# Optimization experiments

Hardware: AMD Instinct MI355X
Metric: run time of the kernel (lower is better)

Reference implementation:

```python
import jax, jax.numpy as jnp
import numpy as np
from jax import lax

DN = ('NCHW', 'OIHW', 'NCHW')

def conv(x, w, b, stride=1, pad=0):
    y = lax.conv_general_dilated(x, w, (stride, stride), ((pad, pad), (pad, pad)), dimension_numbers=DN)
    return y + b[None, :, None, None]

def conv_transpose(x, w, b):
    # torch ConvTranspose2d(k=4, s=2, p=1): w is (in_ch, out_ch, 4, 4)
    wf = jnp.flip(w, (2, 3)).transpose(1, 0, 2, 3)  # -> (out_ch, in_ch, 4, 4)
    pad = 4 - 1 - 1  # k - 1 - p = 2
    y = lax.conv_general_dilated(x, wf, (1, 1), ((pad, pad), (pad, pad)), lhs_dilation=(2, 2), dimension_numbers=DN)
    return y + b[None, :, None, None]

def setup_inputs() -> dict:
    key = jax.random.key(0)
    ks = jax.random.split(key, 16)
    HID, ZC, K = 256, 64, 512
    def w(k, shape):
        return (jax.random.normal(k, shape, jnp.float32) * 0.02)
    z = lambda n: jnp.zeros((n,), jnp.float32)
    return {
        'x': jax.random.uniform(ks[0], (8, 3, 128, 128), jnp.float32),
        'c1_w': w(ks[1], (HID, 3, 4, 4)), 'c1_b': z(HID),
        'c2_w': w(ks[2], (HID, HID, 4, 4)), 'c2_b': z(HID),
        'r0_w3': w(ks[3], (HID, HID, 3, 3)), 'r0_b3': z(HID),
        'r0_w1': w(ks[4], (HID, HID, 1, 1)), 'r0_b1': z(HID),
        'r1_w3': w(ks[5], (HID, HID, 3, 3)), 'r1_b3': z(HID),
        'r1_w1': w(ks[6], (HID, HID, 1, 1)), 'r1_b1': z(HID),
        'to_z_w': w(ks[7], (ZC, HID, 1, 1)), 'to_z_b': z(ZC),
        'codebook': jax.random.uniform(ks[8], (K, ZC), jnp.float32, -1.0 / K, 1.0 / K),
        'from_z_w': w(ks[9], (HID, ZC, 1, 1)), 'from_z_b': z(HID),
        't1_w': w(ks[10], (HID, HID, 4, 4)), 't1_b': z(HID),
        't2_w': w(ks[11], (HID, 3, 4, 4)), 't2_b': z(3),
    }

def _vqvae(x, c1_w, c1_b, c2_w, c2_b, r0_w3, r0_b3, r0_w1, r0_b1,
           r1_w3, r1_b3, r1_w1, r1_b1, to_z_w, to_z_b, codebook,
           from_z_w, from_z_b, t1_w, t1_b, t2_w, t2_b):
    # ---- Encoder ----
    h = jax.nn.relu(conv(x, c1_w, c1_b, stride=2, pad=1))
    h = jax.nn.relu(conv(h, c2_w, c2_b, stride=2, pad=1))
    for (w3, b3, w1, b1) in ((r0_w3, r0_b3, r0_w1, r0_b1), (r1_w3, r1_b3, r1_w1, r1_b1)):
        r = conv(jax.nn.relu(h), w3, b3, pad=1)
        r = conv(jax.nn.relu(r), w1, b1)
        h = h + r
    z_e = conv(h, to_z_w, to_z_b)  # [B, ZC, H/4, W/4]
    # ---- Vector quantization ----
    B, C, H, W = z_e.shape
    z_flat = z_e.transpose(0, 2, 3, 1).reshape(-1, C)  # [N, C]
    dist = (jnp.sum(z_flat * z_flat, axis=1, keepdims=True)
            - 2.0 * z_flat @ codebook.T
            + jnp.sum(codebook * codebook, axis=1)[None, :])  # [N, K]
    ids = jnp.argmin(dist, axis=1)  # [N]
    e_k_flat = codebook[ids]  # [N, C]
    e_k_st_flat = z_flat + lax.stop_gradient(e_k_flat - z_flat)
    e_k = e_k_flat.reshape(B, H, W, C).transpose(0, 3, 1, 2)
    e_k_st = e_k_st_flat.reshape(B, H, W, C).transpose(0, 3, 1, 2)
    ids = ids.reshape(B, H, W)
    # ---- Decoder ----
    d = jax.nn.relu(conv(e_k_st, from_z_w, from_z_b))
    d = jax.nn.relu(conv_transpose(d, t1_w, t1_b))
    out = jax.nn.sigmoid(conv_transpose(d, t2_w, t2_b))
    return out, z_e, e_k, ids

def reference(x, c1_w, c1_b, c2_w, c2_b, r0_w3, r0_b3, r0_w1, r0_b1,
              r1_w3, r1_b3, r1_w1, r1_b1, to_z_w, to_z_b, codebook,
              from_z_w, from_z_b, t1_w, t1_b, t2_w, t2_b):
    return _vqvae(x, c1_w, c1_b, c2_w, c2_b, r0_w3, r0_b3, r0_w1, r0_b1,
                  r1_w3, r1_b3, r1_w1, r1_b1, to_z_w, to_z_b, codebook,
                  from_z_w, from_z_b, t1_w, t1_b, t2_w, t2_b)
```

## Files before the change

kernel.cpp:

```cpp
#include <hip/hip_runtime.h>
#include <math.h>


typedef unsigned int uint;
typedef unsigned short ushort_t;
using short8 = __attribute__((ext_vector_type(8))) short;
using f32x4  = __attribute__((ext_vector_type(4))) float;

__device__ __attribute__((aligned(16))) ushort_t g_zpad[512];

static __device__ __forceinline__ int rfl(int x) { return __builtin_amdgcn_readfirstlane(x); }
static __device__ __forceinline__ ushort_t f2bf(float f) {
  uint u = __float_as_uint(f);
  return (ushort_t)((u + 0x7fffu + ((u >> 16) & 1u)) >> 16);
}
static __device__ __forceinline__ float bf2f(ushort_t b) {
  return __uint_as_float(((uint)b) << 16);
}
static __device__ __forceinline__ void gload16(const ushort_t* g, void* l) {
  __builtin_amdgcn_global_load_lds(
      (const __attribute__((address_space(1))) void*)g,
      (__attribute__((address_space(3))) void*)l, 16, 0, 0);
}

__global__ __launch_bounds__(256) void k_prep_misc(
    const float* __restrict__ c1w, float* __restrict__ wt_c1,
    const float* __restrict__ tozw, float* __restrict__ wt_toz,
    const float* __restrict__ fromzw, float* __restrict__ wt_fromz,
    const float* __restrict__ cb, float* __restrict__ cnorm,
    const float* __restrict__ t2w, ushort_t* __restrict__ w2pk)
{
  const int b = blockIdx.x, tid = threadIdx.x;
  if (b < 48) {
    int idx = b * 256 + tid;
    int co = idx % 256, i = idx / 256;
    wt_c1[idx] = c1w[co * 48 + i];
  } else if (b < 112) {
    int idx = (b - 48) * 256 + tid;
    int co = idx % 64, i = idx / 64;
    wt_toz[idx] = tozw[co * 256 + i];
  } else if (b < 176) {
    int idx = (b - 112) * 256 + tid;
    int co = idx % 256, i = idx / 256;
    wt_fromz[idx] = fromzw[co * 64 + i];
  } else if (b < 178) {
    int idx = (b - 176) * 256 + tid;
    if (idx < 512) {
      float s = 0.f;
      for (int c = 0; c < 64; ++c) { float v = cb[idx * 64 + c]; s = fmaf(v, v, s); }
      cnorm[idx] = s;
    }
  } else {
    int idx = (b - 178) * 256 + tid;
    int k = idx & 31, co = (idx >> 5) & 15, chunk = (idx >> 9) & 31, par = idx >> 14;
    int tap = chunk >> 3, cg = chunk & 7;
    int a = tap >> 1, bb = tap & 1;
    int ry = par & 1, rx = (par >> 1) & 1;
    int ky = ((ry + 1) & 1) + 2 * a;
    int kx = ((rx + 1) & 1) + 2 * bb;
    int ci = cg * 32 + k;
    float v = (co < 3) ? t2w[((ci * 3 + co) << 4) + ky * 4 + kx] : 0.f;
    w2pk[idx] = f2bf(v);
  }
}

template<int KIND>
__global__ __launch_bounds__(256) void k_prep_enc(
    const float* __restrict__ w, ushort_t* __restrict__ wp)
{
  constexpr int KK = (KIND == 0) ? 16 : (KIND == 1 ? 9 : 1);
  constexpr int KW = (KIND == 0) ? 4  : (KIND == 1 ? 3 : 1);
  constexpr int NT = KK;
  const int tid = threadIdx.x;
  const int wvg = blockIdx.x * 4 + (tid >> 6);
  const int lane = tid & 63;
  const int co = wvg >> 2;
  const int ci = (wvg & 3) * 64 + lane;
  const float* src = w + (size_t)(co * 256 + ci) * KK;
  const int coT = co >> 6, row = co & 63, cg = ci >> 5, k = ci & 31;
  float v[KK];
#pragma unroll
  for (int j = 0; j < KK; ++j) v[j] = src[j];
#pragma unroll
  for (int tap = 0; tap < NT; ++tap) {
    int ky, kx;
    if (KIND == 0)      { ky = tap >> 2; kx = tap & 3; }
    else if (KIND == 1) { ky = tap / 3;  kx = tap - ky * 3; }
    else                { ky = 0; kx = 0; }
    float val = v[ky * KW + kx];
    ushort_t b0 = f2bf(val);
    ushort_t b1 = f2bf(val - bf2f(b0));
    const int chunk = tap * 8 + cg;
    size_t base = ((size_t)(chunk * 4 + coT) << 12) + row * 32 + k;
    wp[base] = b0;
    wp[base + 2048] = b1;
  }
}

template<int KIND>
__global__ __launch_bounds__(256) void k_prep_enc2(
    const float* __restrict__ wa, ushort_t* __restrict__ oa,
    const float* __restrict__ wb2, ushort_t* __restrict__ ob)
{
  constexpr int KK = (KIND == 0) ? 16 : (KIND == 1 ? 9 : 1);
  constexpr int KW = (KIND == 0) ? 4  : (KIND == 1 ? 3 : 1);
  constexpr int NT = KK;
  const float* w = (blockIdx.x < 256) ? wa : wb2;
  ushort_t* wp = (blockIdx.x < 256) ? oa : ob;
  const int bx = blockIdx.x & 255;
  const int tid = threadIdx.x;
  const int wvg = bx * 4 + (tid >> 6);
  const int lane = tid & 63;
  const int co = wvg >> 2;
  const int ci = (wvg & 3) * 64 + lane;
  const float* src = w + (size_t)(co * 256 + ci) * KK;
  const int coT = co >> 6, row = co & 63, cg = ci >> 5, k = ci & 31;
  float v[KK];
#pragma unroll
  for (int j = 0; j < KK; ++j) v[j] = src[j];
#pragma unroll
  for (int tap = 0; tap < NT; ++tap) {
    int ky, kx;
    if (KIND == 0)      { ky = tap >> 2; kx = tap & 3; }
    else if (KIND == 1) { ky = tap / 3;  kx = tap - ky * 3; }
    else                { ky = 0; kx = 0; }
    float val = v[ky * KW + kx];
    ushort_t b0 = f2bf(val);
    ushort_t b1 = f2bf(val - bf2f(b0));
    const int chunk = tap * 8 + cg;
    size_t base = ((size_t)(chunk * 4 + coT) << 12) + row * 32 + k;
    wp[base] = b0;
    wp[base + 2048] = b1;
  }
}

__global__ void k_prep_t1w(const float* __restrict__ w, ushort_t* __restrict__ wb) {
  int idx = blockIdx.x * 256 + threadIdx.x;
  int kk  = idx & 31;
  int co  = (idx >> 5) & 255;
  int c8  = (idx >> 13) & 7;
  int tap = (idx >> 16) & 3;
  int par = idx >> 18;
  int ry = par & 1, rx = (par >> 1) & 1;
  int a = tap >> 1, b = tap & 1;
  int ky = ((ry + 1) & 1) + 2 * a;
  int kx = ((rx + 1) & 1) + 2 * b;
  int ci = c8 * 32 + kk;
  wb[idx] = f2bf(w[((ci * 256 + co) << 4) + ky * 4 + kx]);
}

__global__ __launch_bounds__(256) void k_conv1_split(
    const float* __restrict__ in, ushort_t* __restrict__ o0, ushort_t* __restrict__ o1,
    const float* __restrict__ wT, const float* __restrict__ bias)
{
  __shared__ float s_in[3 * 360];
  const int tid = threadIdx.x;
  const int lane = tid & 63;
  const int wv = rfl(tid >> 6);
  const int px = lane & 7, py = lane >> 3;
  const int tx = blockIdx.x & 7, ty = blockIdx.x >> 3;
  const int X = tx * 8, Y = ty * 8;
  const int cob = blockIdx.y * 64 + wv * 16;
  const int n = blockIdx.z;
  float acc[16];
#pragma unroll
  for (int i = 0; i < 16; ++i) acc[i] = bias[cob + i];
  const float* inN = in + (size_t)n * 3 * 16384;
  for (int e = tid; e < 3 * 360; e += 256) {
    int col2 = e % 20; int t = e / 20; int row = t % 18; int ci = t / 18;
    int pr = col2 / 10, hc = col2 % 10, ixl = 2 * hc + pr;
    int iy = 2 * Y - 1 + row, ix = 2 * X - 1 + ixl;
    float v = 0.f;
    if (ixl < 18 && (unsigned)iy < 128u && (unsigned)ix < 128u)
      v = inN[ci * 16384 + iy * 128 + ix];
    s_in[e] = v;
  }
  __syncthreads();
  const float* wc = wT + cob;
#pragma unroll
  for (int c = 0; c < 3; ++c) {
    const float* base = s_in + c * 360 + py * 40 + px;
#pragma unroll
    for (int ky = 0; ky < 4; ++ky) {
#pragma unroll
      for (int kx = 0; kx < 4; ++kx) {
        float iv = base[ky * 20 + (kx & 1) * 10 + (kx >> 1)];
        const float* w = wc + (size_t)(c * 16 + ky * 4 + kx) * 256;
#pragma unroll
        for (int i = 0; i < 16; ++i) acc[i] = fmaf(iv, w[i], acc[i]);
      }
    }
  }
  const int pxg = n * 4096 + (Y + py) * 64 + (X + px);
  uint p0[8], p1[8];
#pragma unroll
  for (int i = 0; i < 8; ++i) {
    float va = fmaxf(acc[2 * i], 0.f), vb = fmaxf(acc[2 * i + 1], 0.f);
    ushort_t a0 = f2bf(va), b0 = f2bf(vb);
    ushort_t a1 = f2bf(va - bf2f(a0)), b1 = f2bf(vb - bf2f(b0));
    p0[i] = (uint)a0 | ((uint)b0 << 16);
    p1[i] = (uint)a1 | ((uint)b1 << 16);
  }
  ushort_t* d0 = o0 + (size_t)pxg * 256 + cob;
  ushort_t* d1 = o1 + (size_t)pxg * 256 + cob;
  uint4 v0a; v0a.x = p0[0]; v0a.y = p0[1]; v0a.z = p0[2]; v0a.w = p0[3];
  uint4 v0b; v0b.x = p0[4]; v0b.y = p0[5]; v0b.z = p0[6]; v0b.w = p0[7];
  uint4 v1a; v1a.x = p1[0]; v1a.y = p1[1]; v1a.z = p1[2]; v1a.w = p1[3];
  uint4 v1b; v1b.x = p1[4]; v1b.y = p1[5]; v1b.z = p1[6]; v1b.w = p1[7];
  *(uint4*)d0 = v0a; *(uint4*)(d0 + 8) = v0b;
  *(uint4*)d1 = v1a; *(uint4*)(d1 + 8) = v1b;
}

template<int KIND>
__global__ __launch_bounds__(256) void k_enc_mfma_split(
    const ushort_t* __restrict__ x0, const ushort_t* __restrict__ x1,
    const ushort_t* __restrict__ wp, float* __restrict__ part)
{
  __shared__ ushort_t smem[2][12288];
  const int tid = threadIdx.x, lane = tid & 63, wv = tid >> 6;
  const int l15 = lane & 15, q = lane >> 4;
  const int pxT = blockIdx.x, coT = blockIdx.y;
  constexpr int NCH = (KIND == 0) ? 128 : 72;
  const int CH0 = blockIdx.z * (NCH / 2), CH1 = CH0 + NCH / 2;
  f32x4 acc[4][2];
#pragma unroll
  for (int m = 0; m < 4; ++m)
#pragma unroll
    for (int n = 0; n < 2; ++n) acc[m][n] = (f32x4){0.f, 0.f, 0.f, 0.f};

  const int r0 = tid >> 2, kq = tid & 3;
  int bimg[2], bu[2], bvc[2];
#pragma unroll
  for (int r = 0; r < 2; ++r) {
    int bpx = pxT * 128 + r0 + r * 64;
    bimg[r] = bpx >> 10; int bp = bpx & 1023; bu[r] = bp >> 5; bvc[r] = bp & 31;
  }
  const ushort_t* srcB[2][2];
  int ptap = -1;
  auto retap = [&](int tap) {
    ptap = tap;
    int ky, kx;
    if (KIND == 0) { ky = tap >> 2; kx = tap & 3; }
    else           { ky = tap / 3;  kx = tap - ky * 3; }
#pragma unroll
    for (int r = 0; r < 2; ++r) {
      bool v; size_t rowb;
      if (KIND == 0) {
        int iy = 2 * bu[r] - 1 + ky, ix = 2 * bvc[r] - 1 + kx;
        v = ((unsigned)iy < 64u) && ((unsigned)ix < 64u);
        rowb = ((size_t)(bimg[r] * 4096 + iy * 64 + ix)) << 8;
      } else {
        int iy = bu[r] - 1 + ky, ix = bvc[r] - 1 + kx;
        v = ((unsigned)iy < 32u) && ((unsigned)ix < 32u);
        rowb = ((size_t)(bimg[r] * 1024 + iy * 32 + ix)) << 8;
      }
      srcB[r][0] = (v ? (x0 + rowb) : g_zpad) + kq * 8;
      srcB[r][1] = (v ? (x1 + rowb) : g_zpad) + kq * 8;
    }
  };

  const int wvb = wv * 1024;
  auto stage = [&](int chunk, int bi) {
    const int tap = chunk >> 3, cg = chunk & 7;
    if (tap != ptap) retap(tap);
    char* bufb = (char*)smem[bi];
    const ushort_t* ap = wp + ((size_t)(chunk * 4 + coT) << 12) + tid * 8;
    gload16(ap,        bufb + wvb);
    gload16(ap + 2048, bufb + 4096 + wvb);
    const int ko = cg * 32;
    gload16(srcB[0][0] + ko, bufb + 8192 + wvb);
    gload16(srcB[1][0] + ko, bufb + 8192 + 4096 + wvb);
    gload16(srcB[0][1] + ko, bufb + 16384 + wvb);
    gload16(srcB[1][1] + ko, bufb + 16384 + 4096 + wvb);
  };
  auto compute = [&](const ushort_t* buf) {
    const ushort_t* sA = buf;
    const ushort_t* sB = buf + 4096;
    short8 af[4][2], bf[2][2];
#pragma unroll
    for (int m = 0; m < 4; ++m)
#pragma unroll
      for (int pl = 0; pl < 2; ++pl)
        af[m][pl] = *(const short8*)(sA + pl * 2048 + (m * 16 + l15) * 32 + q * 8);
#pragma unroll
    for (int n = 0; n < 2; ++n)
#pragma unroll
      for (int pl = 0; pl < 2; ++pl)
        bf[n][pl] = *(const short8*)(sB + pl * 4096 + (wv * 32 + n * 16 + l15) * 32 + q * 8);
#pragma unroll
    for (int m = 0; m < 4; ++m)
#pragma unroll
      for (int n = 0; n < 2; ++n) {
        acc[m][n] = __builtin_amdgcn_mfma_f32_16x16x32_bf16(af[m][0], bf[n][0], acc[m][n], 0, 0, 0);
        acc[m][n] = __builtin_amdgcn_mfma_f32_16x16x32_bf16(af[m][0], bf[n][1], acc[m][n], 0, 0, 0);
        acc[m][n] = __builtin_amdgcn_mfma_f32_16x16x32_bf16(af[m][1], bf[n][0], acc[m][n], 0, 0, 0);
      }
  };

  stage(CH0, 0);
  __syncthreads();
  int cur = 0;
  for (int c = CH0; c < CH1; ++c) {
    if (c + 1 < CH1) stage(c + 1, cur ^ 1);
    compute(smem[cur]);
    __syncthreads();
    cur ^= 1;
  }

  float* pz = part + ((size_t)blockIdx.z << 21);
#pragma unroll
  for (int m = 0; m < 4; ++m) {
#pragma unroll
    for (int n = 0; n < 2; ++n) {
#pragma unroll
      for (int r = 0; r < 4; ++r) {
        const int co_l = m * 16 + q * 4 + r;
        const int px_l = wv * 32 + n * 16 + l15;
        const int px = pxT * 128 + px_l;
        const int img = px >> 10, pp = px & 1023;
        const size_t ha = ((size_t)(img * 256 + coT * 64 + co_l)) * 1024 + pp;
        pz[ha] = acc[m][n][r];
      }
    }
  }
}

__global__ __launch_bounds__(256) void k_enc_mfma_3x3f(
    const ushort_t* __restrict__ x0, const ushort_t* __restrict__ x1,
    const ushort_t* __restrict__ wp, const float* __restrict__ bias,
    ushort_t* __restrict__ s0, ushort_t* __restrict__ s1)
{
  __shared__ ushort_t smem[32768];
  const int tid = threadIdx.x, lane = tid & 63, wv = tid >> 6;
  const int l15 = lane & 15, q = lane >> 4;
  const int pxT = blockIdx.x, coT = blockIdx.y;
  const int img = pxT >> 3;
  const int U0 = (pxT & 7) * 4;
  f32x4 acc[2][2];
#pragma unroll
  for (int m = 0; m < 2; ++m)
#pragma unroll
    for (int n = 0; n < 2; ++n) acc[m][n] = (f32x4){0.f, 0.f, 0.f, 0.f};

  const ushort_t* srcp[7];
#pragma unroll
  for (int i = 0; i < 7; ++i) {
    int slot = i * 256 + tid;
    int pl = slot >= 816 ? 1 : 0;
    int rem = slot - pl * 816;
    int rr = rem / 136;
    int c4 = rem - rr * 136;
    int cc = c4 >> 2, kq2 = c4 & 3;
    int iy = U0 - 1 + rr, ix = cc - 1;
    bool valid = (slot < 1632) && ((unsigned)iy < 32u) && ((unsigned)ix < 32u);
    const ushort_t* base = valid
        ? ((pl ? x1 : x0) + (((size_t)(img * 1024 + iy * 32 + ix)) << 8))
        : g_zpad;
    srcp[i] = base + kq2 * 8;
  }
  const int apl = tid >> 7;
  const int aus = apl * 2048 + (coT & 1) * 1024 + (tid & 127) * 8;
  const int coTq = coT >> 1;
  const int wvb = wv * 1024;
  char* bufb = (char*)smem;

  for (int cg = 0; cg < 8; ++cg) {
#pragma unroll
    for (int tap = 0; tap < 9; ++tap) {
      const int chunk = tap * 8 + cg;
      gload16(wp + ((size_t)(chunk * 4 + coTq) << 12) + aus, bufb + tap * 4096 + wvb);
    }
    const int ko = cg * 32;
#pragma unroll
    for (int i = 0; i < 7; ++i)
      gload16(srcp[i] + ko, bufb + 36864 + i * 4096 + wvb);
    __syncthreads();
    const ushort_t* Ab = smem;
    const ushort_t* Hb = smem + 18432;
#pragma unroll 3
    for (int tap = 0; tap < 9; ++tap) {
      const int ky = tap / 3, kx = tap - ky * 3;
      short8 af[2][2], bf[2][2];
#pragma unroll
      for (int m = 0; m < 2; ++m)
#pragma unroll
        for (int pl = 0; pl < 2; ++pl)
          af[m][pl] = *(const short8*)(Ab + tap * 2048 + pl * 1024 + (m * 16 + l15) * 32 + q * 8);
      const int r = wv + ky;
#pragma unroll
      for (int n = 0; n < 2; ++n)
#pragma unroll
        for (int pl = 0; pl < 2; ++pl)
          bf[n][pl] = *(const short8*)(Hb + pl * 6528 + r * 1088 + (n * 16 + l15 + kx) * 32 + q * 8);
#pragma unroll
      for (int m = 0; m < 2; ++m)
#pragma unroll
        for (int n = 0; n < 2; ++n) {
          acc[m][n] = __builtin_amdgcn_mfma_f32_16x16x32_bf16(af[m][0], bf[n][0], acc[m][n], 0, 0, 0);
          acc[m][n] = __builtin_amdgcn_mfma_f32_16x16x32_bf16(af[m][0], bf[n][1], acc[m][n], 0, 0, 0);
          acc[m][n] = __builtin_amdgcn_mfma_f32_16x16x32_bf16(af[m][1], bf[n][0], acc[m][n], 0, 0, 0);
        }
    }
    __syncthreads();
  }

  const int cob = coT * 32;
#pragma unroll
  for (int m = 0; m < 2; ++m) {
#pragma unroll
    for (int n = 0; n < 2; ++n) {
#pragma unroll
      for (int r = 0; r < 4; ++r) {
        const int co_l = m * 16 + q * 4 + r;
        const int px_l = wv * 32 + n * 16 + l15;
        float sv = fmaxf(acc[m][n][r] + bias[cob + co_l], 0.f);
        ushort_t b0 = f2bf(sv);
        smem[px_l * 32 + co_l] = b0;
        smem[4096 + px_l * 32 + co_l] = f2bf(sv - bf2f(b0));
      }
    }
  }
  __syncthreads();
#pragma unroll
  for (int i = 0; i < 4; ++i) {
    int idx = tid + 256 * i;
    int pl = idx >> 9;
    int rem = idx & 511;
    int px_l = rem >> 2, g = rem & 3;
    uint4 vv = *(const uint4*)(smem + pl * 4096 + px_l * 32 + g * 8);
    ushort_t* dst = (pl ? s1 : s0) + ((size_t)(pxT * 128 + px_l)) * 256 + cob + g * 8;
    *(uint4*)dst = vv;
  }
}

template<bool WH>
__global__ __launch_bounds__(256) void k_enc_epi(
    const float* __restrict__ part, float* __restrict__ h32,
    ushort_t* __restrict__ s0, ushort_t* __restrict__ s1,
    const float* __restrict__ bias)
{
  const int px = blockIdx.x * 256 + threadIdx.x;
  const int co0 = blockIdx.y * 16;
  const int img = px >> 10, pp = px & 1023;
  const float* part1 = part + (1u << 21);
  uint p0[8], p1[8];
#pragma unroll
  for (int i = 0; i < 8; ++i) {
    size_t ha = ((size_t)(img * 256 + co0 + 2 * i)) * 1024 + pp;
    size_t hb = ha + 1024;
    float va = part[ha] + part1[ha] + bias[co0 + 2 * i];
    float vb = part[hb] + part1[hb] + bias[co0 + 2 * i + 1];
    float sa, sb;
    if (WH) {
      va = fmaxf(va, 0.f); vb = fmaxf(vb, 0.f);
      h32[ha] = va; h32[hb] = vb; sa = va; sb = vb;
    } else { sa = fmaxf(va, 0.f); sb = fmaxf(vb, 0.f); }
    ushort_t a0 = f2bf(sa), b0 = f2bf(sb);
    p0[i] = (uint)a0 | ((uint)b0 << 16);
    p1[i] = (uint)f2bf(sa - bf2f(a0)) | ((uint)f2bf(sb - bf2f(b0)) << 16);
  }
  ushort_t* d0 = s0 + (size_t)px * 256 + co0;
  ushort_t* d1 = s1 + (size_t)px * 256 + co0;
  uint4 v0a; v0a.x = p0[0]; v0a.y = p0[1]; v0a.z = p0[2]; v0a.w = p0[3];
  uint4 v0b; v0b.x = p0[4]; v0b.y = p0[5]; v0b.z = p0[6]; v0b.w = p0[7];
  uint4 v1a; v1a.x = p1[0]; v1a.y = p1[1]; v1a.z = p1[2]; v1a.w = p1[3];
  uint4 v1b; v1b.x = p1[4]; v1b.y = p1[5]; v1b.z = p1[6]; v1b.w = p1[7];
  *(uint4*)d0 = v0a; *(uint4*)(d0 + 8) = v0b;
  *(uint4*)d1 = v1a; *(uint4*)(d1 + 8) = v1b;
}

template<bool WS>
__global__ __launch_bounds__(256) void k_enc_mfma(
    const ushort_t* __restrict__ x0, const ushort_t* __restrict__ x1,
    const ushort_t* __restrict__ wp, const float* __restrict__ bias,
    float* __restrict__ h32, ushort_t* __restrict__ sp0, ushort_t* __restrict__ sp1)
{
  __shared__ ushort_t smem[24576];
  const int tid = threadIdx.x, lane = tid & 63, wv = tid >> 6;
  const int l15 = lane & 15, q = lane >> 4;
  const int pxT = blockIdx.x, coT = blockIdx.y;
  f32x4 acc[4][2];
#pragma unroll
  for (int m = 0; m < 4; ++m)
#pragma unroll
    for (int n = 0; n < 2; ++n) acc[m][n] = (f32x4){0.f, 0.f, 0.f, 0.f};

  const int r0 = tid >> 2, kq = tid & 3;
  const ushort_t* srcB[2][2];
#pragma unroll
  for (int r = 0; r < 2; ++r) {
    size_t rowb = ((size_t)(pxT * 128 + r0 + r * 64)) << 8;
    srcB[r][0] = x0 + rowb + kq * 8;
    srcB[r][1] = x1 + rowb + kq * 8;
  }
  const int wvb = wv * 1024;
  auto stage = [&](int c, int bi) {
    char* bufb = (char*)(smem + bi * 12288);
    const ushort_t* ap = wp + ((size_t)(c * 4 + coT) << 12) + tid * 8;
    gload16(ap,        bufb + wvb);
    gload16(ap + 2048, bufb + 4096 + wvb);
    const int ko = c * 32;
    gload16(srcB[0][0] + ko, bufb + 8192 + wvb);
    gload16(srcB[1][0] + ko, bufb + 8192 + 4096 + wvb);
    gload16(srcB[0][1] + ko, bufb + 16384 + wvb);
    gload16(srcB[1][1] + ko, bufb + 16384 + 4096 + wvb);
  };
  auto compute = [&](const ushort_t* buf) {
    const ushort_t* sA = buf;
    const ushort_t* sB = buf + 4096;
    short8 af[4][2], bf[2][2];
#pragma unroll
    for (int m = 0; m < 4; ++m)
#pragma unroll
      for (int pl = 0; pl < 2; ++pl)
        af[m][pl] = *(const short8*)(sA + pl * 2048 + (m * 16 + l15) * 32 + q * 8);
#pragma unroll
    for (int n = 0; n < 2; ++n)
#pragma unroll
      for (int pl = 0; pl < 2; ++pl)
        bf[n][pl] = *(const short8*)(sB + pl * 4096 + (wv * 32 + n * 16 + l15) * 32 + q * 8);
#pragma unroll
    for (int m = 0; m < 4; ++m)
#pragma unroll
      for (int n = 0; n < 2; ++n) {
        acc[m][n] = __builtin_amdgcn_mfma_f32_16x16x32_bf16(af[m][0], bf[n][0], acc[m][n], 0, 0, 0);
        acc[m][n] = __builtin_amdgcn_mfma_f32_16x16x32_bf16(af[m][0], bf[n][1], acc[m][n], 0, 0, 0);
        acc[m][n] = __builtin_amdgcn_mfma_f32_16x16x32_bf16(af[m][1], bf[n][0], acc[m][n], 0, 0, 0);
      }
  };

  stage(0, 0);
  __syncthreads();
  int cur = 0;
  for (int c = 0; c < 8; ++c) {
    if (c + 1 < 8) stage(c + 1, cur ^ 1);
    compute(smem + cur * 12288);
    __syncthreads();
    cur ^= 1;
  }

#pragma unroll
  for (int m = 0; m < 4; ++m) {
#pragma unroll
    for (int n = 0; n < 2; ++n) {
#pragma unroll
      for (int r = 0; r < 4; ++r) {
        const int co_l = m * 16 + q * 4 + r;
        const int px_l = wv * 32 + n * 16 + l15;
        float v = acc[m][n][r] + bias[coT * 64 + co_l];
        const int px = pxT * 128 + px_l;
        const int img = px >> 10, pp = px & 1023;
        const size_t ha = ((size_t)(img * 256 + coT * 64 + co_l)) * 1024 + pp;
        v += h32[ha];
        h32[ha] = v;
        if (WS) {
          float sv = fmaxf(v, 0.f);
          ushort_t b0 = f2bf(sv);
          smem[px_l * 72 + co_l] = b0;
          smem[9216 + px_l * 72 + co_l] = f2bf(sv - bf2f(b0));
        }
      }
    }
  }
  if (WS) {
    __syncthreads();
#pragma unroll
    for (int i = 0; i < 8; ++i) {
      int idx = tid + 256 * i;
      int pl = idx >> 10, w2 = idx & 1023, pxl = w2 >> 3, g = w2 & 7;
      uint4 vv = *(const uint4*)(smem + pl * 9216 + pxl * 72 + g * 8);
      ushort_t* dst = (pl ? sp1 : sp0) + ((size_t)(pxT * 128 + pxl)) * 256 + coT * 64 + g * 8;
      *(uint4*)dst = vv;
    }
  }
}

__global__ __launch_bounds__(256) void k_conv1x1(
    const float* __restrict__ in, float* __restrict__ out,
    const float* __restrict__ wT, const float* __restrict__ bias,
    int CI, int CO, int P)
{
  const int p = blockIdx.x * 256 + threadIdx.x;
  const int cob = blockIdx.y * 16;
  const int n = blockIdx.z;
  const float* inN = in + (size_t)n * CI * P + p;
  float acc[16];
#pragma unroll
  for (int i = 0; i < 16; ++i) acc[i] = bias[cob + i];
  const float* wr = wT + cob;
#pragma unroll 4
  for (int ci = 0; ci < CI; ++ci) {
    float iv = inN[(size_t)ci * P];
    const float* w = wr + (size_t)ci * CO;
#pragma unroll
    for (int i = 0; i < 16; ++i) acc[i] = fmaf(iv, w[i], acc[i]);
  }
  float* outN = out + (size_t)n * CO * P + p;
#pragma unroll
  for (int i = 0; i < 16; ++i) outN[(size_t)(cob + i) * P] = acc[i];
}

__global__ __launch_bounds__(256) void k_vq_part(
    const float* __restrict__ z_e, const float* __restrict__ cb,
    const float* __restrict__ cnorm, float* __restrict__ pbest, int* __restrict__ pbid)
{
  int g = blockIdx.x * 256 + threadIdx.x;
  int chunk = blockIdx.y;
  int img = g >> 10, p = g & 1023;
  const float* zp = z_e + (size_t)img * 64 * 1024 + p;
  float z[64];
#pragma unroll
  for (int c = 0; c < 64; ++c) z[c] = zp[(size_t)c * 1024];
  float best = 3.4e38f; int bid = chunk << 5;
  const int j0 = chunk << 5;
  for (int j = j0; j < j0 + 32; ++j) {
    const float* cj = cb + j * 64;
    float m = 0.f;
#pragma unroll
    for (int c = 0; c < 64; ++c) m = fmaf(z[c], cj[c], m);
    float d = fmaf(-2.f, m, cnorm[j]);
    if (d < best) { best = d; bid = j; }
  }
  pbest[chunk * 8192 + g] = best;
  pbid[chunk * 8192 + g] = bid;
}

__global__ __launch_bounds__(256) void k_vq_reduce(
    const float* __restrict__ pbest, const int* __restrict__ pbid,
    const float* __restrict__ cb, float* __restrict__ ids_f, float* __restrict__ ek)
{
  int g = blockIdx.x * 256 + threadIdx.x;
  float best = 3.4e38f; int bid = 0;
#pragma unroll
  for (int ch = 0; ch < 16; ++ch) {
    float d = pbest[ch * 8192 + g];
    int b = pbid[ch * 8192 + g];
    if (d < best) { best = d; bid = b; }
  }
  ids_f[g] = (float)bid;
  int img = g >> 10, p = g & 1023;
  const float* cbid = cb + bid * 64;
  float* ekp = ek + (size_t)img * 64 * 1024 + p;
#pragma unroll
  for (int c = 0; c < 64; ++c) ekp[(size_t)c * 1024] = cbid[c];
}

__global__ __launch_bounds__(256) void k_from_z(
    const float* __restrict__ ek, ushort_t* __restrict__ nhwc,
    const float* __restrict__ wT, const float* __restrict__ bias)
{
  const int p = blockIdx.x * 256 + threadIdx.x;
  const int co0 = blockIdx.y * 16;
  const int n = blockIdx.z;
  const float* inN = ek + (size_t)n * 64 * 1024 + p;
  float acc[16];
#pragma unroll
  for (int i = 0; i < 16; ++i) acc[i] = bias[co0 + i];
#pragma unroll 4
  for (int ci = 0; ci < 64; ++ci) {
    float iv = inN[(size_t)ci * 1024];
    const float* w = wT + (size_t)ci * 256 + co0;
#pragma unroll
    for (int i = 0; i < 16; ++i) acc[i] = fmaf(iv, w[i], acc[i]);
  }
  uint pk[8];
#pragma unroll
  for (int i = 0; i < 8; ++i) {
    ushort_t lo = f2bf(fmaxf(acc[2 * i], 0.f));
    ushort_t hi = f2bf(fmaxf(acc[2 * i + 1], 0.f));
    pk[i] = (uint)lo | ((uint)hi << 16);
  }
  ushort_t* op = nhwc + (((size_t)n * 1024 + p) * 256 + co0);
  uint4 v0; v0.x = pk[0]; v0.y = pk[1]; v0.z = pk[2]; v0.w = pk[3];
  uint4 v1; v1.x = pk[4]; v1.y = pk[5]; v1.z = pk[6]; v1.w = pk[7];
  *(uint4*)(op) = v0;
  *(uint4*)(op + 8) = v1;
}

__global__ __launch_bounds__(256) void k_mfma_t1(
    const ushort_t* __restrict__ nhwc, const ushort_t* __restrict__ wb,
    const float* __restrict__ bias, ushort_t* __restrict__ t1o)
{
  __shared__ ushort_t smem[24576];
  const int tid = threadIdx.x;
  const int lane = tid & 63;
  const int wv = tid >> 6;
  const int wm = wv & 1, wn = wv >> 1;
  const int l15 = lane & 15, q = lane >> 4;
  const int pxT = blockIdx.x, coT = blockIdx.y, par = blockIdx.z;
  const int ry = par & 1, rx = (par >> 1) & 1;
  const int pxbase = pxT * 128;
  const int img = pxbase >> 10;
  const int U0 = (pxT & 7) * 4;
  f32x4 acc[4][4];
#pragma unroll
  for (int i = 0; i < 4; ++i)
#pragma unroll
    for (int j = 0; j < 4; ++j) acc[i][j] = (f32x4){0.f, 0.f, 0.f, 0.f};

  const ushort_t* srcp[4];
#pragma unroll
  for (int i = 0; i < 4; ++i) {
    int slot = i * 256 + tid;
    int rr = slot / 136;
    int c4 = slot - rr * 136;
    int cc = c4 >> 2, kq2 = c4 & 3;
    int iy = U0 - 1 + rr, ix = cc - 1;
    bool valid = (slot < 816) && ((unsigned)iy < 32u) && ((unsigned)ix < 32u);
    const ushort_t* base = valid
        ? (nhwc + (((size_t)(img * 1024 + iy * 32 + ix)) << 8))
        : g_zpad;
    srcp[i] = base + kq2 * 8;
  }
  const int wvb = wv * 1024;
  char* bufb = (char*)smem;

  for (int c8 = 0; c8 < 8; ++c8) {
#pragma unroll
    for (int tap = 0; tap < 4; ++tap) {
      const ushort_t* Ab = wb + ((size_t)((par * 4 + tap) * 8 + c8) << 13)
                           + coT * 4096 + tid * 8;
      gload16(Ab,        bufb + tap * 8192 + wvb);
      gload16(Ab + 2048, bufb + tap * 8192 + 4096 + wvb);
    }
    const int ko = c8 * 32;
#pragma unroll
    for (int i = 0; i < 4; ++i)
      gload16(srcp[i] + ko, bufb + 32768 + i * 4096 + wvb);
    __syncthreads();
    const ushort_t* A = smem;
    const ushort_t* H = smem + 16384;
#pragma unroll
    for (int tap = 0; tap < 4; ++tap) {
      const int a = tap >> 1, b = tap & 1;
      const int dr = ry + 1 - a, dc = rx + 1 - b;
      short8 af[4], bfr[4];
#pragma unroll
      for (int i = 0; i < 4; ++i)
        af[i] = *(const short8*)(A + tap * 4096 + (wm * 64 + i * 16 + l15) * 32 + q * 8);
#pragma unroll
      for (int j = 0; j < 4; ++j) {
        const int row = wn * 64 + j * 16 + l15;
        const int rr = (row >> 5) + dr, cc = (row & 31) + dc;
        bfr[j] = *(const short8*)(H + rr * 1088 + cc * 32 + q * 8);
      }
#pragma unroll
      for (int i = 0; i < 4; ++i)
#pragma unroll
        for (int j = 0; j < 4; ++j)
          acc[i][j] = __builtin_amdgcn_mfma_f32_16x16x32_bf16(af[i], bfr[j], acc[i][j], 0, 0, 0);
    }
    __syncthreads();
  }

#pragma unroll
  for (int i = 0; i < 4; ++i) {
    int co = coT * 128 + wm * 64 + i * 16 + q * 4;
#pragma unroll
    for (int j = 0; j < 4; ++j) {
      int px = pxbase + wn * 64 + j * 16 + l15;
      int u = (px >> 5) & 31, vv = px & 31;
      int oy = 2 * u + ry, ox = 2 * vv + rx;
      ushort_t e0 = f2bf(fmaxf(acc[i][j][0] + bias[co + 0], 0.f));
      ushort_t e1 = f2bf(fmaxf(acc[i][j][1] + bias[co + 1], 0.f));
      ushort_t e2 = f2bf(fmaxf(acc[i][j][2] + bias[co + 2], 0.f));
      ushort_t e3 = f2bf(fmaxf(acc[i][j][3] + bias[co + 3], 0.f));
      uint2 pk; pk.x = (uint)e0 | ((uint)e1 << 16); pk.y = (uint)e2 | ((uint)e3 << 16);
      *(uint2*)(t1o + ((size_t)(img * 4096 + oy * 64 + ox) * 256 + co)) = pk;
    }
  }
}

__global__ __launch_bounds__(256) void k_mfma_t2(
    const ushort_t* __restrict__ t1o, const ushort_t* __restrict__ wb,
    const float* __restrict__ bias, float* __restrict__ out)
{
  __shared__ ushort_t smem[2][8704];
  const int tid = threadIdx.x, lane = tid & 63, wv = tid >> 6;
  const int l15 = lane & 15, q = lane >> 4;
  const int pxb = blockIdx.x * 256;
  const int par = blockIdx.y;
  const int ry = par & 1, rx = (par >> 1) & 1;
  f32x4 acc[4];
#pragma unroll
  for (int m = 0; m < 4; ++m) acc[m] = (f32x4){0.f, 0.f, 0.f, 0.f};
  const int kg = tid & 3;
  const ushort_t* srcA[4];
  int ptap = -1;
  auto retap = [&](int tap) {
    ptap = tap;
    const int a = tap >> 1, b = tap & 1;
#pragma unroll
    for (int i = 0; i < 4; ++i) {
      int row = (tid >> 2) + 64 * i;
      int px = pxb + row;
      int img = px >> 12, p = px & 4095, u = p >> 6, v = p & 63;
      int iy = u + ry - a, ix = v + rx - b;
      bool valid = ((unsigned)iy < 64u) && ((unsigned)ix < 64u);
      srcA[i] = (valid ? (t1o + (((size_t)(img * 4096 + iy * 64 + ix)) << 8)) : g_zpad)
                + kg * 8;
    }
  };
  const int wvb = wv * 1024;
  auto stage = [&](int c, int bi) {
    const int tap = c >> 3, cg = c & 7;
    if (tap != ptap) retap(tap);
    char* bufb = (char*)smem[bi];
    const int ko = cg * 32;
#pragma unroll
    for (int i = 0; i < 4; ++i)
      gload16(srcA[i] + ko, bufb + i * 4096 + wvb);
    if (tid < 64)
      gload16(wb + ((size_t)(par * 32 + c)) * 512 + tid * 8, bufb + 16384);
  };
  auto compute = [&](const ushort_t* buf) {
    const ushort_t* sA = buf;
    const ushort_t* sB = buf + 8192;
    short8 bf = *(const short8*)(sB + l15 * 32 + q * 8);
#pragma unroll
    for (int m = 0; m < 4; ++m) {
      const int row = wv * 64 + m * 16 + l15;
      short8 af = *(const short8*)(sA + row * 32 + q * 8);
      acc[m] = __builtin_amdgcn_mfma_f32_16x16x32_bf16(af, bf, acc[m], 0, 0, 0);
    }
  };

  stage(0, 0);
  __syncthreads();
  int cur = 0;
  for (int c = 0; c < 32; ++c) {
    if (c + 1 < 32) stage(c + 1, cur ^ 1);
    compute(smem[cur]);
    __syncthreads();
    cur ^= 1;
  }

  const int co = l15;
  if (co < 3) {
    float bco = bias[co];
#pragma unroll
    for (int m = 0; m < 4; ++m) {
#pragma unroll
      for (int r = 0; r < 4; ++r) {
        int px = pxb + wv * 64 + m * 16 + q * 4 + r;
        int img = px >> 12, p = px & 4095, u = p >> 6, v = p & 63;
        size_t addr = ((size_t)(img * 3 + co)) * 16384 + (2 * u + ry) * 128 + (2 * v + rx);
        out[addr] = 1.f / (1.f + expf(-(acc[m][r] + bco)));
      }
    }
  }
}

extern "C" void kernel_launch(void* const* d_in, const int* in_sizes, int n_in,
                              void* d_out, int out_size, void* d_ws, size_t ws_size,
                              hipStream_t stream) {
  (void)in_sizes; (void)n_in; (void)out_size; (void)ws_size;
  const float* x      = (const float*)d_in[0];
  const float* c1_w   = (const float*)d_in[1];
  const float* c1_b   = (const float*)d_in[2];
  const float* c2_w   = (const float*)d_in[3];
  const float* c2_b   = (const float*)d_in[4];
  const float* r0_w3  = (const float*)d_in[5];
  const float* r0_b3  = (const float*)d_in[6];
  const float* r0_w1  = (const float*)d_in[7];
  const float* r0_b1  = (const float*)d_in[8];
  const float* r1_w3  = (const float*)d_in[9];
  const float* r1_b3  = (const float*)d_in[10];
  const float* r1_w1  = (const float*)d_in[11];
  const float* r1_b1  = (const float*)d_in[12];
  const float* to_z_w = (const float*)d_in[13];
  const float* to_z_b = (const float*)d_in[14];
  const float* cb     = (const float*)d_in[15];
  const float* from_z_w = (const float*)d_in[16];
  const float* from_z_b = (const float*)d_in[17];
  const float* t1_w   = (const float*)d_in[18];
  const float* t1_b   = (const float*)d_in[19];
  const float* t2_w   = (const float*)d_in[20];
  const float* t2_b   = (const float*)d_in[21];

  float* wsf = (float*)d_ws;
  ushort_t* xs1p0 = (ushort_t*)(wsf + 0);
  ushort_t* xs1p1 = (ushort_t*)(wsf + 4194304);
  float*    cp0   = wsf + 8388608;
  float*    h32   = wsf + 8388608;
  ushort_t* sE0   = (ushort_t*)(wsf + 0);
  ushort_t* sE1   = (ushort_t*)(wsf + 1048576);
  ushort_t* sF0   = (ushort_t*)(wsf + 2097152);
  ushort_t* sF1   = (ushort_t*)(wsf + 3145728);
  float*    pbest = wsf + 0;
  int*      pbid  = (int*)(wsf + 131072);
  ushort_t* t1out = (ushort_t*)(wsf + 2097152);
  ushort_t* decn  = (ushort_t*)(wsf + 6291456);
  ushort_t* wp_c2   = (ushort_t*)(wsf + 12582912);
  ushort_t* wp_r0w3 = (ushort_t*)(wsf + 13631488);
  ushort_t* wp_r1w3 = (ushort_t*)(wsf + 14221312);
  ushort_t* wp_r0w1 = (ushort_t*)(wsf + 14811136);
  ushort_t* wp_r1w1 = (ushort_t*)(wsf + 14876672);
  float*    wt_c1   = wsf + 14942208;
  float*    wt_toz  = wsf + 14954496;
  float*    wt_fromz= wsf + 14970880;
  ushort_t* t1wb    = (ushort_t*)(wsf + 14987264);
  ushort_t* w2pk    = (ushort_t*)(wsf + 15511552);
  float*    cnorm   = wsf + 15544320;

  float* out_img = (float*)d_out;
  float* z_e_out = out_img + 393216;
  float* e_k_out = z_e_out + 524288;
  float* ids_out = e_k_out + 524288;

  k_prep_misc<<<434, 256, 0, stream>>>(c1_w, wt_c1, to_z_w, wt_toz,
                                       from_z_w, wt_fromz, cb, cnorm, t2_w, w2pk);
  k_prep_enc<0><<<256, 256, 0, stream>>>(c2_w, wp_c2);
  k_prep_enc2<1><<<512, 256, 0, stream>>>(r0_w3, wp_r0w3, r1_w3, wp_r1w3);
  k_prep_enc2<2><<<512, 256, 0, stream>>>(r0_w1, wp_r0w1, r1_w1, wp_r1w1);
  k_prep_t1w<<<4096, 256, 0, stream>>>(t1_w, t1wb);

  k_conv1_split<<<dim3(64, 4, 8), 256, 0, stream>>>(x, xs1p0, xs1p1, wt_c1, c1_b);
  k_enc_mfma_split<0><<<dim3(64, 4, 2), 256, 0, stream>>>(xs1p0, xs1p1, wp_c2, cp0);
  k_enc_epi<true><<<dim3(32, 16), 256, 0, stream>>>(cp0, h32, sE0, sE1, c2_b);
  k_enc_mfma_3x3f<<<dim3(64, 8), 256, 0, stream>>>(sE0, sE1, wp_r0w3, r0_b3, sF0, sF1);
  k_enc_mfma<true ><<<dim3(64, 4), 256, 0, stream>>>(
      sF0, sF1, wp_r0w1, r0_b1, h32, sE0, sE1);
  k_enc_mfma_3x3f<<<dim3(64, 8), 256, 0, stream>>>(sE0, sE1, wp_r1w3, r1_b3, sF0, sF1);
  k_enc_mfma<false><<<dim3(64, 4), 256, 0, stream>>>(
      sF0, sF1, wp_r1w1, r1_b1, h32, nullptr, nullptr);
  k_conv1x1<<<dim3(4, 4, 8), 256, 0, stream>>>(h32, z_e_out, wt_toz, to_z_b, 256, 64, 1024);

  k_vq_part<<<dim3(32, 16), 256, 0, stream>>>(z_e_out, cb, cnorm, pbest, pbid);
  k_vq_reduce<<<32, 256, 0, stream>>>(pbest, pbid, cb, ids_out, e_k_out);

  k_from_z<<<dim3(4, 16, 8), 256, 0, stream>>>(e_k_out, decn, wt_fromz, from_z_b);
  k_mfma_t1<<<dim3(64, 2, 4), 256, 0, stream>>>(decn, t1wb, t1_b, t1out);
  k_mfma_t2<<<dim3(128, 4), 256, 0, stream>>>(t1out, w2pk, t2_b, out_img);
}
```

Measured before the change: 392.2 us.

## Merge weight-prep kernels and halve output tiles of 1x1 convs for more blocks

Four weight-preparation launches are merged into one kernel dispatched by block range, which removes launch overhead. The 1x1 MFMA encoder conv now computes 32 output channels per block instead of 64, doubling the grid to 512 blocks and shrinking LDS use. The scalar to_z 1x1 conv likewise handles 8 channels per block instead of 16, doubling its grid. The trade is more occupancy and parallelism in exchange for reloading the activation tiles twice as often.

```diff
diff --git a/kernel.cpp b/kernel.cpp
--- a/kernel.cpp
+++ b/kernel.cpp
@@ -23,56 +23,14 @@
       (__attribute__((address_space(3))) void*)l, 16, 0, 0);
 }
 
-__global__ __launch_bounds__(256) void k_prep_misc(
-    const float* __restrict__ c1w, float* __restrict__ wt_c1,
-    const float* __restrict__ tozw, float* __restrict__ wt_toz,
-    const float* __restrict__ fromzw, float* __restrict__ wt_fromz,
-    const float* __restrict__ cb, float* __restrict__ cnorm,
-    const float* __restrict__ t2w, ushort_t* __restrict__ w2pk)
-{
-  const int b = blockIdx.x, tid = threadIdx.x;
-  if (b < 48) {
-    int idx = b * 256 + tid;
-    int co = idx % 256, i = idx / 256;
-    wt_c1[idx] = c1w[co * 48 + i];
-  } else if (b < 112) {
-    int idx = (b - 48) * 256 + tid;
-    int co = idx % 64, i = idx / 64;
-    wt_toz[idx] = tozw[co * 256 + i];
-  } else if (b < 176) {
-    int idx = (b - 112) * 256 + tid;
-    int co = idx % 256, i = idx / 256;
-    wt_fromz[idx] = fromzw[co * 64 + i];
-  } else if (b < 178) {
-    int idx = (b - 176) * 256 + tid;
-    if (idx < 512) {
-      float s = 0.f;
-      for (int c = 0; c < 64; ++c) { float v = cb[idx * 64 + c]; s = fmaf(v, v, s); }
-      cnorm[idx] = s;
-    }
-  } else {
-    int idx = (b - 178) * 256 + tid;
-    int k = idx & 31, co = (idx >> 5) & 15, chunk = (idx >> 9) & 31, par = idx >> 14;
-    int tap = chunk >> 3, cg = chunk & 7;
-    int a = tap >> 1, bb = tap & 1;
-    int ry = par & 1, rx = (par >> 1) & 1;
-    int ky = ((ry + 1) & 1) + 2 * a;
-    int kx = ((rx + 1) & 1) + 2 * bb;
-    int ci = cg * 32 + k;
-    float v = (co < 3) ? t2w[((ci * 3 + co) << 4) + ky * 4 + kx] : 0.f;
-    w2pk[idx] = f2bf(v);
-  }
-}
-
 template<int KIND>
-__global__ __launch_bounds__(256) void k_prep_enc(
-    const float* __restrict__ w, ushort_t* __restrict__ wp)
+static __device__ __forceinline__ void d_prep_enc_body(
+    int bx, int tid, const float* __restrict__ w, ushort_t* __restrict__ wp)
 {
   constexpr int KK = (KIND == 0) ? 16 : (KIND == 1 ? 9 : 1);
   constexpr int KW = (KIND == 0) ? 4  : (KIND == 1 ? 3 : 1);
   constexpr int NT = KK;
-  const int tid = threadIdx.x;
-  const int wvg = blockIdx.x * 4 + (tid >> 6);
+  const int wvg = bx * 4 + (tid >> 6);
   const int lane = tid & 63;
   const int co = wvg >> 2;
   const int ci = (wvg & 3) * 64 + lane;
@@ -97,40 +55,61 @@
   }
 }
 
-template<int KIND>
-__global__ __launch_bounds__(256) void k_prep_enc2(
-    const float* __restrict__ wa, ushort_t* __restrict__ oa,
-    const float* __restrict__ wb2, ushort_t* __restrict__ ob)
-{
-  constexpr int KK = (KIND == 0) ? 16 : (KIND == 1 ? 9 : 1);
-  constexpr int KW = (KIND == 0) ? 4  : (KIND == 1 ? 3 : 1);
-  constexpr int NT = KK;
-  const float* w = (blockIdx.x < 256) ? wa : wb2;
-  ushort_t* wp = (blockIdx.x < 256) ? oa : ob;
-  const int bx = blockIdx.x & 255;
-  const int tid = threadIdx.x;
-  const int wvg = bx * 4 + (tid >> 6);
-  const int lane = tid & 63;
-  const int co = wvg >> 2;
-  const int ci = (wvg & 3) * 64 + lane;
-  const float* src = w + (size_t)(co * 256 + ci) * KK;
-  const int coT = co >> 6, row = co & 63, cg = ci >> 5, k = ci & 31;
-  float v[KK];
-#pragma unroll
-  for (int j = 0; j < KK; ++j) v[j] = src[j];
-#pragma unroll
-  for (int tap = 0; tap < NT; ++tap) {
-    int ky, kx;
-    if (KIND == 0)      { ky = tap >> 2; kx = tap & 3; }
-    else if (KIND == 1) { ky = tap / 3;  kx = tap - ky * 3; }
-    else                { ky = 0; kx = 0; }
-    float val = v[ky * KW + kx];
-    ushort_t b0 = f2bf(val);
-    ushort_t b1 = f2bf(val - bf2f(b0));
-    const int chunk = tap * 8 + cg;
-    size_t base = ((size_t)(chunk * 4 + coT) << 12) + row * 32 + k;
-    wp[base] = b0;
-    wp[base + 2048] = b1;
+__global__ __launch_bounds__(256) void k_prep_all(
+    const float* __restrict__ c1w, float* __restrict__ wt_c1,
+    const float* __restrict__ tozw, float* __restrict__ wt_toz,
+    const float* __restrict__ fromzw, float* __restrict__ wt_fromz,
+    const float* __restrict__ cb, float* __restrict__ cnorm,
+    const float* __restrict__ t2w, ushort_t* __restrict__ w2pk,
+    const float* __restrict__ c2w, ushort_t* __restrict__ wp_c2,
+    const float* __restrict__ r0w3, ushort_t* __restrict__ wp_r0w3,
+    const float* __restrict__ r1w3, ushort_t* __restrict__ wp_r1w3,
+    const float* __restrict__ r0w1, ushort_t* __restrict__ wp_r0w1,
+    const float* __restrict__ r1w1, ushort_t* __restrict__ wp_r1w1)
+{
+  const int b = blockIdx.x, tid = threadIdx.x;
+  if (b < 434) {
+    if (b < 48) {
+      int idx = b * 256 + tid;
+      int co = idx % 256, i = idx / 256;
+      wt_c1[idx] = c1w[co * 48 + i];
+    } else if (b < 112) {
+      int idx = (b - 48) * 256 + tid;
+      int co = idx % 64, i = idx / 64;
+      wt_toz[idx] = tozw[co * 256 + i];
+    } else if (b < 176) {
+      int idx = (b - 112) * 256 + tid;
+      int co = idx % 256, i = idx / 256;
+      wt_fromz[idx] = fromzw[co * 64 + i];
+    } else if (b < 178) {
+      int idx = (b - 176) * 256 + tid;
+      if (idx < 512) {
+        float s = 0.f;
+        for (int c = 0; c < 64; ++c) { float v = cb[idx * 64 + c]; s = fmaf(v, v, s); }
+        cnorm[idx] = s;
+      }
+    } else {
+      int idx = (b - 178) * 256 + tid;
+      int k = idx & 31, co = (idx >> 5) & 15, chunk = (idx >> 9) & 31, par = idx >> 14;
+      int tap = chunk >> 3, cg = chunk & 7;
+      int a = tap >> 1, bb = tap & 1;
+      int ry = par & 1, rx = (par >> 1) & 1;
+      int ky = ((ry + 1) & 1) + 2 * a;
+      int kx = ((rx + 1) & 1) + 2 * bb;
+      int ci = cg * 32 + k;
+      float v = (co < 3) ? t2w[((ci * 3 + co) << 4) + ky * 4 + kx] : 0.f;
+      w2pk[idx] = f2bf(v);
+    }
+  } else if (b < 690) {
+    d_prep_enc_body<0>(b - 434, tid, c2w, wp_c2);
+  } else if (b < 1202) {
+    int bx = b - 690;
+    if (bx < 256) d_prep_enc_body<1>(bx, tid, r0w3, wp_r0w3);
+    else          d_prep_enc_body<1>(bx - 256, tid, r1w3, wp_r1w3);
+  } else {
+    int bx = b - 1202;
+    if (bx < 256) d_prep_enc_body<2>(bx, tid, r0w1, wp_r0w1);
+    else          d_prep_enc_body<2>(bx - 256, tid, r1w1, wp_r1w1);
   }
 }
 
@@ -475,13 +454,14 @@
     const ushort_t* __restrict__ wp, const float* __restrict__ bias,
     float* __restrict__ h32, ushort_t* __restrict__ sp0, ushort_t* __restrict__ sp1)
 {
-  __shared__ ushort_t smem[24576];
+  __shared__ ushort_t smem[20480];
   const int tid = threadIdx.x, lane = tid & 63, wv = tid >> 6;
   const int l15 = lane & 15, q = lane >> 4;
   const int pxT = blockIdx.x, coT = blockIdx.y;
-  f32x4 acc[4][2];
-#pragma unroll
-  for (int m = 0; m < 4; ++m)
+  const int coT4 = coT >> 1, half = coT & 1;
+  f32x4 acc[2][2];
+#pragma unroll
+  for (int m = 0; m < 2; ++m)
 #pragma unroll
     for (int n = 0; n < 2; ++n) acc[m][n] = (f32x4){0.f, 0.f, 0.f, 0.f};
 
@@ -493,34 +473,35 @@
     srcB[r][0] = x0 + rowb + kq * 8;
     srcB[r][1] = x1 + rowb + kq * 8;
   }
+  const int apl = wv >> 1, asub = wv & 1;
+  const int aoff = apl * 2048 + half * 1024 + asub * 512 + lane * 8;
   const int wvb = wv * 1024;
   auto stage = [&](int c, int bi) {
-    char* bufb = (char*)(smem + bi * 12288);
-    const ushort_t* ap = wp + ((size_t)(c * 4 + coT) << 12) + tid * 8;
-    gload16(ap,        bufb + wvb);
-    gload16(ap + 2048, bufb + 4096 + wvb);
+    char* bufb = (char*)(smem + bi * 10240);
+    const ushort_t* ap = wp + ((size_t)(c * 4 + coT4) << 12) + aoff;
+    gload16(ap, bufb + wvb);
     const int ko = c * 32;
-    gload16(srcB[0][0] + ko, bufb + 8192 + wvb);
-    gload16(srcB[1][0] + ko, bufb + 8192 + 4096 + wvb);
-    gload16(srcB[0][1] + ko, bufb + 16384 + wvb);
-    gload16(srcB[1][1] + ko, bufb + 16384 + 4096 + wvb);
+    gload16(srcB[0][0] + ko, bufb + 4096 + wvb);
+    gload16(srcB[1][0] + ko, bufb + 8192 + wvb);
+    gload16(srcB[0][1] + ko, bufb + 12288 + wvb);
+    gload16(srcB[1][1] + ko, bufb + 16384 + wvb);
   };
   auto compute = [&](const ushort_t* buf) {
     const ushort_t* sA = buf;
-    const ushort_t* sB = buf + 4096;
-    short8 af[4][2], bf[2][2];
-#pragma unroll
-    for (int m = 0; m < 4; ++m)
+    const ushort_t* sB = buf + 2048;
+    short8 af[2][2], bf[2][2];
+#pragma unroll
+    for (int m = 0; m < 2; ++m)
 #pragma unroll
       for (int pl = 0; pl < 2; ++pl)
-        af[m][pl] = *(const short8*)(sA + pl * 2048 + (m * 16 + l15) * 32 + q * 8);
+        af[m][pl] = *(const short8*)(sA + pl * 1024 + (m * 16 + l15) * 32 + q * 8);
 #pragma unroll
     for (int n = 0; n < 2; ++n)
 #pragma unroll
       for (int pl = 0; pl < 2; ++pl)
         bf[n][pl] = *(const short8*)(sB + pl * 4096 + (wv * 32 + n * 16 + l15) * 32 + q * 8);
 #pragma unroll
-    for (int m = 0; m < 4; ++m)
+    for (int m = 0; m < 2; ++m)
 #pragma unroll
       for (int n = 0; n < 2; ++n) {
         acc[m][n] = __builtin_amdgcn_mfma_f32_16x16x32_bf16(af[m][0], bf[n][0], acc[m][n], 0, 0, 0);
@@ -534,30 +515,31 @@
   int cur = 0;
   for (int c = 0; c < 8; ++c) {
     if (c + 1 < 8) stage(c + 1, cur ^ 1);
-    compute(smem + cur * 12288);
+    compute(smem + cur * 10240);
     __syncthreads();
     cur ^= 1;
   }
 
-#pragma unroll
-  for (int m = 0; m < 4; ++m) {
+  const int cob = coT * 32;
+#pragma unroll
+  for (int m = 0; m < 2; ++m) {
 #pragma unroll
     for (int n = 0; n < 2; ++n) {
 #pragma unroll
       for (int r = 0; r < 4; ++r) {
         const int co_l = m * 16 + q * 4 + r;
         const int px_l = wv * 32 + n * 16 + l15;
-        float v = acc[m][n][r] + bias[coT * 64 + co_l];
+        float v = acc[m][n][r] + bias[cob + co_l];
         const int px = pxT * 128 + px_l;
         const int img = px >> 10, pp = px & 1023;
-        const size_t ha = ((size_t)(img * 256 + coT * 64 + co_l)) * 1024 + pp;
+        const size_t ha = ((size_t)(img * 256 + cob + co_l)) * 1024 + pp;
         v += h32[ha];
         h32[ha] = v;
         if (WS) {
           float sv = fmaxf(v, 0.f);
           ushort_t b0 = f2bf(sv);
-          smem[px_l * 72 + co_l] = b0;
-          smem[9216 + px_l * 72 + co_l] = f2bf(sv - bf2f(b0));
+          smem[px_l * 32 + co_l] = b0;
+          smem[4096 + px_l * 32 + co_l] = f2bf(sv - bf2f(b0));
         }
       }
     }
@@ -565,11 +547,13 @@
   if (WS) {
     __syncthreads();
 #pragma unroll
-    for (int i = 0; i < 8; ++i) {
+    for (int i = 0; i < 4; ++i) {
       int idx = tid + 256 * i;
-      int pl = idx >> 10, w2 = idx & 1023, pxl = w2 >> 3, g = w2 & 7;
-      uint4 vv = *(const uint4*)(smem + pl * 9216 + pxl * 72 + g * 8);
-      ushort_t* dst = (pl ? sp1 : sp0) + ((size_t)(pxT * 128 + pxl)) * 256 + coT * 64 + g * 8;
+      int pl = idx >> 9;
+      int rem = idx & 511;
+      int px_l = rem >> 2, g = rem & 3;
+      uint4 vv = *(const uint4*)(smem + pl * 4096 + px_l * 32 + g * 8);
+      ushort_t* dst = (pl ? sp1 : sp0) + ((size_t)(pxT * 128 + px_l)) * 256 + cob + g * 8;
       *(uint4*)dst = vv;
     }
   }
@@ -581,23 +565,23 @@
     int CI, int CO, int P)
 {
   const int p = blockIdx.x * 256 + threadIdx.x;
-  const int cob = blockIdx.y * 16;
+  const int cob = blockIdx.y * 8;
   const int n = blockIdx.z;
   const float* inN = in + (size_t)n * CI * P + p;
-  float acc[16];
-#pragma unroll
-  for (int i = 0; i < 16; ++i) acc[i] = bias[cob + i];
+  float acc[8];
+#pragma unroll
+  for (int i = 0; i < 8; ++i) acc[i] = bias[cob + i];
   const float* wr = wT + cob;
 #pragma unroll 4
   for (int ci = 0; ci < CI; ++ci) {
     float iv = inN[(size_t)ci * P];
     const float* w = wr + (size_t)ci * CO;
 #pragma unroll
-    for (int i = 0; i < 16; ++i) acc[i] = fmaf(iv, w[i], acc[i]);
+    for (int i = 0; i < 8; ++i) acc[i] = fmaf(iv, w[i], acc[i]);
   }
   float* outN = out + (size_t)n * CO * P + p;
 #pragma unroll
-  for (int i = 0; i < 16; ++i) outN[(size_t)(cob + i) * P] = acc[i];
+  for (int i = 0; i < 8; ++i) outN[(size_t)(cob + i) * P] = acc[i];
 }
 
 __global__ __launch_bounds__(256) void k_vq_part(
@@ -908,23 +892,21 @@
   float* e_k_out = z_e_out + 524288;
   float* ids_out = e_k_out + 524288;
 
-  k_prep_misc<<<434, 256, 0, stream>>>(c1_w, wt_c1, to_z_w, wt_toz,
-                                       from_z_w, wt_fromz, cb, cnorm, t2_w, w2pk);
-  k_prep_enc<0><<<256, 256, 0, stream>>>(c2_w, wp_c2);
-  k_prep_enc2<1><<<512, 256, 0, stream>>>(r0_w3, wp_r0w3, r1_w3, wp_r1w3);
-  k_prep_enc2<2><<<512, 256, 0, stream>>>(r0_w1, wp_r0w1, r1_w1, wp_r1w1);
+  k_prep_all<<<1714, 256, 0, stream>>>(
+      c1_w, wt_c1, to_z_w, wt_toz, from_z_w, wt_fromz, cb, cnorm, t2_w, w2pk,
+      c2_w, wp_c2, r0_w3, wp_r0w3, r1_w3, wp_r1w3, r0_w1, wp_r0w1, r1_w1, wp_r1w1);
   k_prep_t1w<<<4096, 256, 0, stream>>>(t1_w, t1wb);
 
   k_conv1_split<<<dim3(64, 4, 8), 256, 0, stream>>>(x, xs1p0, xs1p1, wt_c1, c1_b);
   k_enc_mfma_split<0><<<dim3(64, 4, 2), 256, 0, stream>>>(xs1p0, xs1p1, wp_c2, cp0);
   k_enc_epi<true><<<dim3(32, 16), 256, 0, stream>>>(cp0, h32, sE0, sE1, c2_b);
   k_enc_mfma_3x3f<<<dim3(64, 8), 256, 0, stream>>>(sE0, sE1, wp_r0w3, r0_b3, sF0, sF1);
-  k_enc_mfma<true ><<<dim3(64, 4), 256, 0, stream>>>(
+  k_enc_mfma<true ><<<dim3(64, 8), 256, 0, stream>>>(
       sF0, sF1, wp_r0w1, r0_b1, h32, sE0, sE1);
   k_enc_mfma_3x3f<<<dim3(64, 8), 256, 0, stream>>>(sE0, sE1, wp_r1w3, r1_b3, sF0, sF1);
-  k_enc_mfma<false><<<dim3(64, 4), 256, 0, stream>>>(
+  k_enc_mfma<false><<<dim3(64, 8), 256, 0, stream>>>(
       sF0, sF1, wp_r1w1, r1_b1, h32, nullptr, nullptr);
-  k_conv1x1<<<dim3(4, 4, 8), 256, 0, stream>>>(h32, z_e_out, wt_toz, to_z_b, 256, 64, 1024);
+  k_conv1x1<<<dim3(4, 8, 8), 256, 0, stream>>>(h32, z_e_out, wt_toz, to_z_b, 256, 64, 1024);
 
   k_vq_part<<<dim3(32, 16), 256, 0, stream>>>(z_e_out, cb, cnorm, pbest, pbid);
   k_vq_reduce<<<32, 256, 0, stream>>>(pbest, pbid, cb, ids_out, e_k_out);
```

After: 370.5 us. 1.06x faster.
